# Kernel tuning notes

Hardware: AMD Instinct MI355X
Metric: run time of the kernel (lower is better)

## Reference

```python
import jax, jax.numpy as jnp
import numpy as np
from jax import lax

NF = 64
RED = 16  # CALayer / CBAM channel reduction


def conv1x1(x, w, b):
    # x: [B,Ci,H,W], w: [Co,Ci], b: [Co]
    return jnp.einsum('oi,bihw->bohw', w, x) + b[None, :, None, None]


def calayer(x, w1, b1, w2, b2):
    # SE-style channel attention (RCAN CALayer): global avg pool -> 1x1 conv -> ReLU -> 1x1 conv -> sigmoid
    y = x.mean(axis=(2, 3))                      # [B,C]
    z = jax.nn.relu(y @ w1.T + b1)               # [B,C//RED]
    s = jax.nn.sigmoid(z @ w2.T + b2)            # [B,C]
    return x * s[:, :, None, None]


def mean_variance_norm(x, eps=1e-5):
    # per-sample, per-channel spatial instance norm (AdaAttN style)
    m = x.mean(axis=(2, 3), keepdims=True)
    v = x.var(axis=(2, 3), keepdims=True)
    return (x - m) / jnp.sqrt(v + eps)


def cbam(x, mlp_w1, mlp_b1, mlp_w2, mlp_b2, sp_w, sp_b):
    # BasicAttentionBlockv1 assumed to be a CBAM block (docstring: "CBAM")
    avg = x.mean(axis=(2, 3))                    # [B,C]
    mx = x.max(axis=(2, 3))                      # [B,C]
    def mlp(v):
        return jax.nn.relu(v @ mlp_w1.T + mlp_b1) @ mlp_w2.T + mlp_b2
    s = jax.nn.sigmoid(mlp(avg) + mlp(mx))       # [B,C]
    x = x * s[:, :, None, None]
    sp_in = jnp.concatenate([x.mean(axis=1, keepdims=True), x.max(axis=1, keepdims=True)], axis=1)  # [B,2,H,W]
    m = lax.conv_general_dilated(sp_in, sp_w, (1, 1), 'SAME',
                                 dimension_numbers=('NCHW', 'OIHW', 'NCHW')) + sp_b[None, :, None, None]
    return x * jax.nn.sigmoid(m)


def setup_inputs() -> dict:
    key = jax.random.key(0)
    ks = iter(jax.random.split(key, 64))
    B, N, C, H, W = 4, 3, NF, 64, 64
    r = lambda shape, s=0.05: jax.random.normal(next(ks), shape, dtype=jnp.float32) * s
    inp = {
        'group': jax.random.normal(next(ks), (B, N, C, H, W), dtype=jnp.float32),
        'FG': jax.random.normal(next(ks), (B, N, C, H, W), dtype=jnp.float32),
        'BG': jax.random.normal(next(ks), (B, N, C, H, W), dtype=jnp.float32),
        # conv_group_1 (3nf->3nf 1x1), CALayer(3nf), conv_group_2 (3nf->nf), conv_group_3 (nf->nf)
        'wg1': r((3 * C, 3 * C)), 'bg1': r((3 * C,)),
        'cag_w1': r((3 * C // RED, 3 * C)), 'cag_b1': r((3 * C // RED,)),
        'cag_w2': r((3 * C, 3 * C // RED)), 'cag_b2': r((3 * C,)),
        'wg2': r((C, 3 * C)), 'bg2': r((C,)),
        'wg3': r((C, C)), 'bg3': r((C,)),
        # conv_center_1, CALayer(nf), conv_center_2
        'wc1': r((C, C)), 'bc1': r((C,)),
        'cac_w1': r((C // RED, C)), 'cac_b1': r((C // RED,)),
        'cac_w2': r((C, C // RED)), 'cac_b2': r((C,)),
        'wc2': r((C, C)), 'bc2': r((C,)),
        # f, g, h 1x1 convs
        'f_w': r((C, C)), 'f_b': r((C,)),
        'g_w': r((C, C)), 'g_b': r((C,)),
        'h_w': r((C, C)), 'h_b': r((C,)),
        # CBAM params
        'mlp_w1': r((C // RED, C)), 'mlp_b1': r((C // RED,)),
        'mlp_w2': r((C, C // RED)), 'mlp_b2': r((C,)),
        'sp_w': r((1, 2, 7, 7)), 'sp_b': r((1,)),
    }
    return inp


def reference(group, FG, BG,
              wg1, bg1, cag_w1, cag_b1, cag_w2, cag_b2, wg2, bg2, wg3, bg3,
              wc1, bc1, cac_w1, cac_b1, cac_w2, cac_b2, wc2, bc2,
              f_w, f_b, g_w, g_b, h_w, h_b,
              mlp_w1, mlp_b1, mlp_w2, mlp_b2, sp_w, sp_b):
    B, N, C, H, W = group.shape
    center = group[:, 1]
    FGc = FG[:, 1]
    BGc = BG[:, 1]
    grp = group.reshape(B, N * C, H, W)

    fea_group = conv1x1(grp, wg1, bg1)
    fea_group = calayer(fea_group, cag_w1, cag_b1, cag_w2, cag_b2)
    fea_group = conv1x1(fea_group, wg2, bg2)
    fea_group = conv1x1(fea_group, wg3, bg3)

    fea_center = conv1x1(center, wc1, bc1)
    fea_center = calayer(fea_center, cac_w1, cac_b1, cac_w2, cac_b2)
    fea_center = conv1x1(fea_center, wc2, bc2)

    Fq = conv1x1(fea_group, f_w, f_b).reshape(B, C, H * W).transpose(0, 2, 1)   # [B,HW,C]
    Gk = conv1x1(fea_center, g_w, g_b).reshape(B, C, H * W)                     # [B,C,HW]
    Hv = conv1x1(BGc, h_w, h_b).reshape(B, C, H * W).transpose(0, 2, 1)         # [B,HW,C]

    S = jax.nn.softmax(jnp.einsum('bqc,bck->bqk', Fq, Gk), axis=-1)             # [B,HW,HW]
    mean = jnp.einsum('bqk,bkc->bqc', S, Hv)                                    # [B,HW,C]
    second = jnp.einsum('bqk,bkc->bqc', S, Hv * Hv)
    std = jnp.sqrt(jax.nn.relu(second - mean * mean))

    mean = mean.reshape(B, H, W, C).transpose(0, 3, 1, 2)
    std = std.reshape(B, H, W, C).transpose(0, 3, 1, 2)

    transfer_FG = std * mean_variance_norm(FGc) + mean
    out = cbam(transfer_FG + BGc, mlp_w1, mlp_b1, mlp_w2, mlp_b2, sp_w, sp_b)
    return out
```

## Files before the change

kernel.cpp:

```cpp
#include <hip/hip_runtime.h>
#include <hip/hip_bf16.h>
#include <math.h>

#define HW 4096

typedef __attribute__((ext_vector_type(8))) short bf16x8;
typedef __attribute__((ext_vector_type(4))) float f32x4;

static __device__ __forceinline__ unsigned short f2bf(float x) {
    unsigned u = __float_as_uint(x);
    u += 0x7fffu + ((u >> 16) & 1u);
    return (unsigned short)(u >> 16);
}
static __device__ __forceinline__ float bf2f(unsigned short h) {
    return __uint_as_float((unsigned)h << 16);
}

__global__ __launch_bounds__(256) void k_transpose2(
    const float* __restrict__ group, const float* __restrict__ BGc, int bstride,
    unsigned short* __restrict__ X0T, unsigned short* __restrict__ BGcT)
{
    extern __shared__ float lds[];
    const int b = blockIdx.y, p0 = blockIdx.x << 6, t = threadIdx.x;
    const int z = blockIdx.z;
    const int C = z ? 64 : 192;
    const float* xb = (z ? BGc : group) + (size_t)b * bstride;
    unsigned short* outT = z ? BGcT : X0T;
    for (int idx = t; idx < (C << 6); idx += 256) {
        int c = idx >> 6, p = idx & 63;
        lds[c * 65 + p] = xb[(size_t)c * HW + p0 + p];
    }
    __syncthreads();
    unsigned short* ob = outT + ((size_t)b * HW + p0) * C;
    for (int idx = t; idx < (C << 6); idx += 256) {
        int p = idx / C, c = idx - p * C;
        ob[idx] = f2bf(lds[c * 65 + p]);
    }
}

__global__ __launch_bounds__(256) void k_xmean(
    const float* __restrict__ g, int bstride, float* __restrict__ xmean)
{
    int bc = blockIdx.x;
    int b = bc / 192, ci = bc - b * 192;
    const float* p = g + (size_t)b * bstride + (size_t)ci * HW;
    int t = threadIdx.x;
    float s = 0.f;
    for (int i = t; i < HW; i += 256) s += p[i];
    for (int o = 32; o > 0; o >>= 1) s += __shfl_down(s, o, 64);
    __shared__ float red[4];
    if ((t & 63) == 0) red[t >> 6] = s;
    __syncthreads();
    if (t == 0) xmean[bc] = (red[0] + red[1] + red[2] + red[3]) * (1.0f / HW);
}

__global__ __launch_bounds__(256) void k_mlp_compose(
    const float* __restrict__ xmean,
    const float* __restrict__ wg1, const float* __restrict__ bg1,
    const float* __restrict__ cag_w1, const float* __restrict__ cag_b1,
    const float* __restrict__ cag_w2, const float* __restrict__ cag_b2,
    const float* __restrict__ wc1, const float* __restrict__ bc1,
    const float* __restrict__ cac_w1, const float* __restrict__ cac_b1,
    const float* __restrict__ cac_w2, const float* __restrict__ cac_b2,
    const float* __restrict__ wg2, const float* __restrict__ bg2,
    const float* __restrict__ wg3, const float* __restrict__ bg3,
    const float* __restrict__ wc2, const float* __restrict__ bc2,
    const float* __restrict__ wf, const float* __restrict__ fb,
    const float* __restrict__ wgw, const float* __restrict__ gbv,
    const float* __restrict__ wh,
    unsigned short* __restrict__ WQb, float* __restrict__ biasQ,
    unsigned short* __restrict__ WKb, float* __restrict__ biasK,
    unsigned short* __restrict__ whb)
{
    const float LOG2E = 1.4426950408889634f;
    __shared__ float SM[29184];
    float* xm = SM;
    float* sg = SM + 192;
    float* sc = SM + 384;
    float* zz = SM + 448;
    float* T1 = SM + 512;
    float* Aa = SM + 4608;
    float* W1S = SM + 16896;
    float* Mm = SM + 26112;
    const int x = blockIdx.x, b = blockIdx.y, t = threadIdx.x;

    if (t < 192) xm[t] = xmean[b * 192 + t];
    __syncthreads();
    if (t < 192) {
        float a = bg1[t];
        for (int i = 0; i < 192; ++i) a = fmaf(wg1[t * 192 + i], xm[i], a);
        sg[t] = a;
    } else {
        int c = t - 192;
        float a = bc1[c];
        for (int i = 0; i < 64; ++i) a = fmaf(wc1[c * 64 + i], xm[64 + i], a);
        sc[c] = a;
    }
    __syncthreads();
    if (t < 12) {
        float a = cag_b1[t];
        for (int i = 0; i < 192; ++i) a = fmaf(cag_w1[t * 192 + i], sg[i], a);
        zz[t] = fmaxf(a, 0.f);
    }
    if (t >= 64 && t < 68) {
        int r = t - 64;
        float a = cac_b1[r];
        for (int i = 0; i < 64; ++i) a = fmaf(cac_w1[r * 64 + i], sc[i], a);
        zz[12 + r] = fmaxf(a, 0.f);
    }
    __syncthreads();
    if (t < 192) {
        float a = cag_b2[t];
        for (int j = 0; j < 12; ++j) a = fmaf(cag_w2[t * 12 + j], zz[j], a);
        sg[t] = 1.f / (1.f + __expf(-a));
    } else {
        int c = t - 192;
        float a = cac_b2[c];
        for (int j = 0; j < 4; ++j) a = fmaf(cac_w2[c * 4 + j], zz[12 + j], a);
        sc[c] = 1.f / (1.f + __expf(-a));
    }
    __syncthreads();
    float* wfS = Aa;
    float* wg3S = Aa + 4096;
    #pragma unroll
    for (int j = 0; j < 16; ++j) {
        wfS[t + j * 256] = wf[t + j * 256];
        wg3S[t + j * 256] = wg3[t + j * 256];
    }
    __syncthreads();
    #pragma unroll
    for (int j = 0; j < 16; ++j) {
        int idx = t + j * 256, o = idx >> 6, k = idx & 63;
        float a = 0.f;
        for (int m = 0; m < 64; ++m) a = fmaf(wfS[(o << 6) + m], wg3S[(m << 6) + k], a);
        T1[idx] = a;
    }
    __syncthreads();
    for (int idx = t; idx < 12288; idx += 256)
        Aa[idx] = wg2[idx] * sg[idx % 192];
    const int i0 = x * 48;
    for (int idx = t; idx < 9216; idx += 256) {
        int r = idx / 48, ii = idx - r * 48;
        W1S[idx] = wg1[r * 192 + i0 + ii];
    }
    __syncthreads();
    for (int idx = t; idx < 3072; idx += 256) {
        int o = idx / 48, ii = idx - o * 48;
        float a = 0.f;
        for (int k = 0; k < 192; ++k) a = fmaf(Aa[o * 192 + k], W1S[k * 48 + ii], a);
        Mm[idx] = a;
    }
    __syncthreads();
    for (int idx = t; idx < 3072; idx += 256) {
        int o = idx / 48, ii = idx - o * 48;
        float a = 0.f;
        for (int m = 0; m < 64; ++m) a = fmaf(T1[(o << 6) + m], Mm[m * 48 + ii], a);
        WQb[(size_t)b * 12288 + o * 192 + i0 + ii] = f2bf(a * LOG2E);
    }

    if (x == 0) {
        float* bq1 = Mm;
        float* bq2 = Mm + 64;
        float* bk1 = Mm + 128;
        __syncthreads();
        if (t < 64) {
            float a = bg2[t];
            for (int i = 0; i < 192; ++i) a = fmaf(Aa[t * 192 + i], bg1[i], a);
            bq1[t] = a;
            float c = bc2[t];
            for (int j = 0; j < 64; ++j) c = fmaf(wc2[t * 64 + j] * sc[j], bc1[j], c);
            bk1[t] = c;
        }
        __syncthreads();
        if (t < 64) {
            float a = bg3[t];
            for (int m = 0; m < 64; ++m) a = fmaf(wg3[t * 64 + m], bq1[m], a);
            bq2[t] = a;
        }
        __syncthreads();
        if (t < 64) {
            float a = fb[t];
            for (int m = 0; m < 64; ++m) a = fmaf(wf[t * 64 + m], bq2[m], a);
            biasQ[b * 64 + t] = a * LOG2E;
            float c = gbv[t];
            for (int m = 0; m < 64; ++m) c = fmaf(wgw[t * 64 + m], bk1[m], c);
            biasK[b * 64 + t] = c;
        }
        float* wc1S = Aa;
        float* wc2S = Aa + 4096;
        float* T3   = Aa + 8192;
        __syncthreads();
        #pragma unroll
        for (int j = 0; j < 16; ++j) {
            int idx = t + j * 256;
            wc1S[idx] = wc1[idx];
            wc2S[idx] = wc2[idx] * sc[idx & 63];
        }
        __syncthreads();
        #pragma unroll
        for (int j = 0; j < 16; ++j) {
            int idx = t + j * 256, m = idx >> 6, i = idx & 63;
            float a = 0.f;
            for (int k = 0; k < 64; ++k) a = fmaf(wc2S[(m << 6) + k], wc1S[(k << 6) + i], a);
            T3[idx] = a;
        }
        __syncthreads();
        #pragma unroll
        for (int j = 0; j < 16; ++j) {
            int idx = t + j * 256, o = idx >> 6, i = idx & 63;
            float a = 0.f;
            for (int m = 0; m < 64; ++m) a = fmaf(wgw[(o << 6) + m], T3[(m << 6) + i], a);
            WKb[(size_t)b * 4096 + idx] = f2bf(a);
        }
        if (b == 0) {
            #pragma unroll
            for (int j = 0; j < 16; ++j) whb[t + j * 256] = f2bf(wh[t + j * 256]);
        }
    }
}

__global__ __launch_bounds__(256) void k_proj(
    const unsigned short* __restrict__ X0T, const unsigned short* __restrict__ BGcT,
    const unsigned short* __restrict__ WQb, const float* __restrict__ biasQ,
    const unsigned short* __restrict__ WKb, const float* __restrict__ biasK,
    const unsigned short* __restrict__ whb, const float* __restrict__ h_b,
    unsigned short* __restrict__ FqT, unsigned short* __restrict__ GkT,
    unsigned short* __restrict__ hvN)
{
    const int t = threadIdx.x;
    const int w = t >> 6, lane = t & 63;
    const int gid = lane >> 4, cid = lane & 15;
    const int which = blockIdx.y;
    const int b = blockIdx.z;
    const int p0 = blockIdx.x << 6;
    const int co16 = w << 4;
    int Cin, kOff, ldx;
    const unsigned short *XT, *W;
    const float* bp;
    if (which == 0) { XT = X0T; ldx = 192; kOff = 0;  Cin = 192; W = WQb + (size_t)b * 12288; bp = biasQ + b * 64; }
    else if (which == 1) { XT = X0T; ldx = 192; kOff = 64; Cin = 64; W = WKb + (size_t)b * 4096; bp = biasK + b * 64; }
    else { XT = BGcT; ldx = 64; kOff = 0; Cin = 64; W = whb; bp = h_b; }
    const unsigned short* xrow = XT + (size_t)b * HW * ldx + kOff;
    const unsigned short* wr = W + (size_t)co16 * Cin;
    f32x4 acc[4];
    #pragma unroll
    for (int n = 0; n < 4; ++n)
        #pragma unroll
        for (int r = 0; r < 4; ++r)
            acc[n][r] = bp[co16 + 4 * gid + r];
    for (int kc = 0; kc < Cin; kc += 32) {
        bf16x8 a = *(const bf16x8*)(wr + (size_t)cid * Cin + kc + 8 * gid);
        #pragma unroll
        for (int n = 0; n < 4; ++n) {
            const unsigned short* xp = xrow + (size_t)(p0 + 16 * n + cid) * ldx + kc + 8 * gid;
            bf16x8 bfr = *(const bf16x8*)xp;
            acc[n] = __builtin_amdgcn_mfma_f32_16x16x32_bf16(a, bfr, acc[n], 0, 0, 0);
        }
    }
    #pragma unroll
    for (int n = 0; n < 4; ++n)
        #pragma unroll
        for (int r = 0; r < 4; ++r) {
            float v = acc[n][r];
            int co = co16 + 4 * gid + r;
            int p  = p0 + 16 * n + cid;
            if (which == 0)      FqT[((size_t)b * HW + p) * 64 + co] = f2bf(v);
            else if (which == 1) GkT[((size_t)b * HW + p) * 64 + co] = f2bf(v);
            else                 hvN[((size_t)b * 64 + co) * HW + p] = f2bf(v);
        }
}

__global__ __launch_bounds__(512, 2) void k_attn(
    const unsigned short* __restrict__ FqT, const unsigned short* __restrict__ GkT,
    const unsigned short* __restrict__ HvN,
    float* __restrict__ mb, float* __restrict__ sbuf)
{
    __shared__ __align__(16) char smem[65536];
    const int t = threadIdx.x;
    const int bid = blockIdx.x;
    const int b = (bid & 7) >> 1;
    const int qbase = (((bid >> 3) << 1) | (bid & 1)) << 6;
    const int w = t >> 6, lane = t & 63;
    const int gid = lane >> 4, cid = lane & 15;
    const size_t CQ = (size_t)HW * 64;
    const unsigned short* fqt = FqT + (size_t)b * CQ;
    const unsigned short* gkt = GkT + (size_t)b * CQ;
    const unsigned short* hv  = HvN + (size_t)b * CQ;
    unsigned short* Pw = (unsigned short*)smem + w * 4096;

    bf16x8 fqa[4][2];
    #pragma unroll
    for (int qt = 0; qt < 4; ++qt) {
        const unsigned short* fr = fqt + (size_t)(qbase + 16 * qt + cid) * 64 + 8 * gid;
        fqa[qt][0] = *(const bf16x8*)fr;
        fqa[qt][1] = *(const bf16x8*)(fr + 32);
    }
    bf16x8 ones;
    #pragma unroll
    for (int j = 0; j < 8; ++j) ones[j] = (short)0x3F80;

    const f32x4 fz = {0.f, 0.f, 0.f, 0.f};
    f32x4 am[4][4], a2[4][4], lac[4];
    #pragma unroll
    for (int qt = 0; qt < 4; ++qt) {
        lac[qt] = fz;
        #pragma unroll
        for (int n = 0; n < 4; ++n) { am[qt][n] = fz; a2[qt][n] = fz; }
    }

    const int k00 = w << 9;
    for (int it = 0; it < 8; ++it) {
        const int k0 = k00 + (it << 6);
        #pragma unroll
        for (int n = 0; n < 4; ++n) {
            const unsigned short* gr = gkt + (size_t)(k0 + 16 * n + cid) * 64 + 8 * gid;
            bf16x8 b0 = *(const bf16x8*)gr;
            bf16x8 b1 = *(const bf16x8*)(gr + 32);
            const int k = 16 * n + cid;
            #pragma unroll
            for (int qt = 0; qt < 4; ++qt) {
                f32x4 s = __builtin_amdgcn_mfma_f32_16x16x32_bf16(fqa[qt][0], b0, fz, 0, 0, 0);
                s = __builtin_amdgcn_mfma_f32_16x16x32_bf16(fqa[qt][1], b1, s, 0, 0, 0);
                #pragma unroll
                for (int r = 0; r < 4; ++r) {
                    int q = 4 * gid + r;
                    Pw[qt * 1024 + q * 64 + (((k >> 3) ^ (q & 7)) << 3) + (k & 7)] =
                        f2bf(__builtin_amdgcn_exp2f(s[r]));
                }
            }
        }
        bf16x8 pa[4][2];
        #pragma unroll
        for (int qt = 0; qt < 4; ++qt)
            #pragma unroll
            for (int kh = 0; kh < 2; ++kh)
                pa[qt][kh] = *(const bf16x8*)(Pw + qt * 1024 + cid * 64 +
                                              (((4 * kh + gid) ^ (cid & 7)) << 3));
        #pragma unroll
        for (int qt = 0; qt < 4; ++qt) {
            lac[qt] = __builtin_amdgcn_mfma_f32_16x16x32_bf16(pa[qt][0], ones, lac[qt], 0, 0, 0);
            lac[qt] = __builtin_amdgcn_mfma_f32_16x16x32_bf16(pa[qt][1], ones, lac[qt], 0, 0, 0);
        }
        #pragma unroll
        for (int n = 0; n < 4; ++n) {
            const unsigned short* hr = hv + (size_t)(16 * n + cid) * HW + k0;
            #pragma unroll
            for (int kh = 0; kh < 2; ++kh) {
                bf16x8 hb = *(const bf16x8*)(hr + 32 * kh + 8 * gid);
                bf16x8 h2;
                #pragma unroll
                for (int j = 0; j < 8; ++j) {
                    float v = bf2f((unsigned short)hb[j]);
                    h2[j] = (short)f2bf(v * v);
                }
                #pragma unroll
                for (int qt = 0; qt < 4; ++qt) {
                    am[qt][n] = __builtin_amdgcn_mfma_f32_16x16x32_bf16(pa[qt][kh], hb, am[qt][n], 0, 0, 0);
                    a2[qt][n] = __builtin_amdgcn_mfma_f32_16x16x32_bf16(pa[qt][kh], h2, a2[qt][n], 0, 0, 0);
                }
            }
        }
    }

    __syncthreads();
    float* lb = (float*)smem;
    #pragma unroll
    for (int qt = 0; qt < 4; ++qt)
        *(f32x4*)(lb + ((size_t)(w * 4 + qt) * 64 + lane) * 4) = lac[qt];
    __syncthreads();
    float* Lm = (float*)(smem + 32768);
    if (t < 256) {
        int qt = t >> 6, ls = t & 63;
        f32x4 s = fz;
        #pragma unroll
        for (int ww = 0; ww < 8; ++ww)
            s += *(const f32x4*)(lb + ((size_t)(ww * 4 + qt) * 64 + ls) * 4);
        *(f32x4*)(Lm + ((size_t)qt * 64 + ls) * 4) = s;
    }
    __syncthreads();
    float* ab = (float*)smem;
    f32x4 meanv = fz;
    for (int qt = 0; qt < 4; ++qt) {
        #pragma unroll
        for (int n = 0; n < 4; ++n)
            *(f32x4*)(ab + ((size_t)(w * 4 + n) * 64 + lane) * 4) = am[qt][n];
        __syncthreads();
        if (t < 256) {
            int n = t >> 6, ls = t & 63;
            f32x4 s = fz;
            #pragma unroll
            for (int ww = 0; ww < 8; ++ww)
                s += *(const f32x4*)(ab + ((size_t)(ww * 4 + n) * 64 + ls) * 4);
            f32x4 lv = *(const f32x4*)(Lm + ((size_t)qt * 64 + ls) * 4);
            #pragma unroll
            for (int r = 0; r < 4; ++r) meanv[r] = s[r] / lv[r];
            int q0s = qbase + 16 * qt + 4 * (ls >> 4);
            int c   = 16 * n + (ls & 15);
            *(f32x4*)(mb + (size_t)b * CQ + (size_t)c * HW + q0s) = meanv;
        }
        __syncthreads();
        #pragma unroll
        for (int n = 0; n < 4; ++n)
            *(f32x4*)(ab + ((size_t)(w * 4 + n) * 64 + lane) * 4) = a2[qt][n];
        __syncthreads();
        if (t < 256) {
            int n = t >> 6, ls = t & 63;
            f32x4 s = fz;
            #pragma unroll
            for (int ww = 0; ww < 8; ++ww)
                s += *(const f32x4*)(ab + ((size_t)(ww * 4 + n) * 64 + ls) * 4);
            f32x4 lv = *(const f32x4*)(Lm + ((size_t)qt * 64 + ls) * 4);
            f32x4 sv;
            #pragma unroll
            for (int r = 0; r < 4; ++r) {
                float sec = s[r] / lv[r];
                sv[r] = sqrtf(fmaxf(sec - meanv[r] * meanv[r], 0.f));
            }
            int q0s = qbase + 16 * qt + 4 * (ls >> 4);
            int c   = 16 * n + (ls & 15);
            *(f32x4*)(sbuf + (size_t)b * CQ + (size_t)c * HW + q0s) = sv;
        }
        __syncthreads();
    }
}

__global__ __launch_bounds__(256) void k_transfer_f(
    const float* __restrict__ mb, const float* __restrict__ sb,
    const float* __restrict__ FG, const float* __restrict__ BG, int bstride,
    float* __restrict__ xb, float* __restrict__ pavg, float* __restrict__ pmaxb)
{
    __shared__ float fgl[4096];
    __shared__ float r1[4], r2[4];
    const int bc = blockIdx.x, t = threadIdx.x;
    const int b = bc >> 6, c = bc & 63;
    const size_t row = (size_t)bc * HW;
    const float* fg = FG + (size_t)b * bstride + (size_t)(64 + c) * HW;
    const float* bg = BG + (size_t)b * bstride + (size_t)(64 + c) * HW;
    float s = 0.f, s2 = 0.f;
    #pragma unroll
    for (int j = 0; j < 16; ++j) {
        int i = t + j * 256;
        float v = fg[i];
        fgl[i] = v;
        s += v; s2 += v * v;
    }
    #pragma unroll
    for (int o = 32; o > 0; o >>= 1) { s += __shfl_down(s, o, 64); s2 += __shfl_down(s2, o, 64); }
    if ((t & 63) == 0) { r1[t >> 6] = s; r2[t >> 6] = s2; }
    __syncthreads();
    float m  = (r1[0] + r1[1] + r1[2] + r1[3]) * (1.0f / HW);
    float e2 = (r2[0] + r2[1] + r2[2] + r2[3]) * (1.0f / HW);
    float rs = rsqrtf(fmaxf(e2 - m * m, 0.f) + 1e-5f);
    float psum = 0.f, pmax = -1e30f;
    #pragma unroll
    for (int j = 0; j < 16; ++j) {
        int q = t + j * 256;
        float xv = sb[row + q] * (fgl[q] - m) * rs + mb[row + q] + bg[q];
        xb[row + q] = xv;
        psum += xv; pmax = fmaxf(pmax, xv);
    }
    __syncthreads();
    #pragma unroll
    for (int o = 32; o > 0; o >>= 1) {
        psum += __shfl_down(psum, o, 64);
        pmax = fmaxf(pmax, __shfl_down(pmax, o, 64));
    }
    if ((t & 63) == 0) { r1[t >> 6] = psum; r2[t >> 6] = pmax; }
    __syncthreads();
    if (t == 0) {
        pavg[bc]  = (r1[0] + r1[1] + r1[2] + r1[3]) * (1.0f / HW);
        pmaxb[bc] = fmaxf(fmaxf(r2[0], r2[1]), fmaxf(r2[2], r2[3]));
    }
}

static __device__ __forceinline__ void cbam_scale(
    const float* __restrict__ pav, const float* __restrict__ pmx,
    const float* __restrict__ w1, const float* __restrict__ b1,
    const float* __restrict__ w2, const float* __restrict__ b2,
    int b, int t, float* scb)
{
    __shared__ float za[4], zm[4];
    if (t < 4) {
        float aa = b1[t], am = b1[t];
        for (int i = 0; i < 64; ++i) {
            aa = fmaf(w1[t * 64 + i], pav[b * 64 + i], aa);
            am = fmaf(w1[t * 64 + i], pmx[b * 64 + i], am);
        }
        za[t] = fmaxf(aa, 0.f);
        zm[t] = fmaxf(am, 0.f);
    }
    __syncthreads();
    if (t < 64) {
        float a = 2.f * b2[t];
        for (int j = 0; j < 4; ++j) a = fmaf(w2[t * 4 + j], za[j] + zm[j], a);
        scb[t] = 1.f / (1.f + __expf(-a));
    }
    __syncthreads();
}

__global__ __launch_bounds__(256) void k_sp_pool(
    const float* __restrict__ xb,
    const float* __restrict__ pav, const float* __restrict__ pmx,
    const float* __restrict__ w1, const float* __restrict__ b1,
    const float* __restrict__ w2, const float* __restrict__ b2,
    float* __restrict__ spm, float* __restrict__ spx)
{
    __shared__ float scb[64];
    const int b = blockIdx.y, t = threadIdx.x;
    cbam_scale(pav, pmx, w1, b1, w2, b2, b, t, scb);
    const int p = blockIdx.x * 256 + t;
    const float* xp = xb + (size_t)b * 262144 + p;
    float sum = 0.f, mx = -1e30f;
    for (int c = 0; c < 64; ++c) {
        float v = xp[(size_t)c * HW] * scb[c];
        sum += v;
        mx = fmaxf(mx, v);
    }
    spm[b * HW + p] = sum * (1.0f / 64.0f);
    spx[b * HW + p] = mx;
}

__global__ __launch_bounds__(256) void k_spf(
    const float* __restrict__ spm, const float* __restrict__ spx,
    const float* __restrict__ w, const float* __restrict__ bias,
    const float* __restrict__ xb,
    const float* __restrict__ pav, const float* __restrict__ pmx,
    const float* __restrict__ w1, const float* __restrict__ b1,
    const float* __restrict__ w2, const float* __restrict__ b2,
    float* __restrict__ out)
{
    __shared__ float scb[64];
    const int b = blockIdx.y, t = threadIdx.x;
    cbam_scale(pav, pmx, w1, b1, w2, b2, b, t, scb);
    const int p = blockIdx.x * 256 + t;
    const int y = p >> 6, x = p & 63;
    float acc = bias[0];
    for (int dy = 0; dy < 7; ++dy) {
        int yy = y + dy - 3;
        if (yy < 0 || yy >= 64) continue;
        for (int dx = 0; dx < 7; ++dx) {
            int xx = x + dx - 3;
            if (xx < 0 || xx >= 64) continue;
            int q = b * HW + yy * 64 + xx;
            acc = fmaf(spm[q], w[dy * 7 + dx],      acc);
            acc = fmaf(spx[q], w[49 + dy * 7 + dx], acc);
        }
    }
    float sgm = 1.f / (1.f + __expf(-acc));
    const float* xp = xb + (size_t)b * 262144 + p;
    float* op = out + (size_t)b * 262144 + p;
    for (int c = 0; c < 64; ++c)
        op[(size_t)c * HW] = xp[(size_t)c * HW] * scb[c] * sgm;
}

extern "C" void kernel_launch(void* const* d_in, const int* in_sizes, int n_in,
                              void* d_out, int out_size, void* d_ws, size_t ws_size,
                              hipStream_t stream)
{
    const float* group  = (const float*)d_in[0];
    const float* FG     = (const float*)d_in[1];
    const float* BG     = (const float*)d_in[2];
    const float* wg1    = (const float*)d_in[3];
    const float* bg1    = (const float*)d_in[4];
    const float* cag_w1 = (const float*)d_in[5];
    const float* cag_b1 = (const float*)d_in[6];
    const float* cag_w2 = (const float*)d_in[7];
    const float* cag_b2 = (const float*)d_in[8];
    const float* wg2    = (const float*)d_in[9];
    const float* bg2    = (const float*)d_in[10];
    const float* wg3    = (const float*)d_in[11];
    const float* bg3    = (const float*)d_in[12];
    const float* wc1    = (const float*)d_in[13];
    const float* bc1    = (const float*)d_in[14];
    const float* cac_w1 = (const float*)d_in[15];
    const float* cac_b1 = (const float*)d_in[16];
    const float* cac_w2 = (const float*)d_in[17];
    const float* cac_b2 = (const float*)d_in[18];
    const float* wc2    = (const float*)d_in[19];
    const float* bc2    = (const float*)d_in[20];
    const float* f_w    = (const float*)d_in[21];
    const float* f_b    = (const float*)d_in[22];
    const float* g_w    = (const float*)d_in[23];
    const float* g_b    = (const float*)d_in[24];
    const float* h_w    = (const float*)d_in[25];
    const float* h_b    = (const float*)d_in[26];
    const float* mlp_w1 = (const float*)d_in[27];
    const float* mlp_b1 = (const float*)d_in[28];
    const float* mlp_w2 = (const float*)d_in[29];
    const float* mlp_b2 = (const float*)d_in[30];
    const float* sp_w   = (const float*)d_in[31];
    const float* sp_b   = (const float*)d_in[32];
    float* out = (float*)d_out;

    const int B = 4;
    const size_t CHW = (size_t)64 * HW;
    const int BST = (int)(3 * CHW);

    float* ws = (float*)d_ws;
    const size_t M = 1048576;
    unsigned short* X0T  = (unsigned short*)ws;
    unsigned short* BGcT = (unsigned short*)(ws + 3 * M / 2);
    unsigned short* FqT  = (unsigned short*)(ws + 2 * M);
    unsigned short* GkT  = (unsigned short*)(ws + 5 * M / 2);
    unsigned short* hvN  = (unsigned short*)(ws + 3 * M);
    float* mbuf = ws + 7 * M / 2;
    float* sbuf = ws + 9 * M / 2;
    float* xb   = ws + 2 * M;
    float* smalls = ws + 11 * M / 2;
    float* xmean = smalls;
    float* pav   = smalls + 1024;
    float* pmx   = smalls + 1280;
    float* biasQ = smalls + 1536;
    float* biasK = smalls + 1792;
    float* spm   = smalls + 2048;
    float* spx   = smalls + 18432;
    unsigned short* wsh = (unsigned short*)(smalls + 34816);
    unsigned short* WQb = wsh;
    unsigned short* WKb = wsh + 49152;
    unsigned short* whb = wsh + 65536;

    dim3 blk(256);

    k_transpose2<<<dim3(64, B, 2), blk, 192 * 65 * 4, stream>>>(group, BG + CHW, BST, X0T, BGcT);
    k_xmean<<<B * 192, blk, 0, stream>>>(group, BST, xmean);
    k_mlp_compose<<<dim3(4, B), blk, 0, stream>>>(
        xmean, wg1, bg1, cag_w1, cag_b1, cag_w2, cag_b2,
        wc1, bc1, cac_w1, cac_b1, cac_w2, cac_b2,
        wg2, bg2, wg3, bg3, wc2, bc2,
        f_w, f_b, g_w, g_b, h_w,
        WQb, biasQ, WKb, biasK, whb);
    k_proj<<<dim3(64, 3, B), blk, 0, stream>>>(
        X0T, BGcT, WQb, biasQ, WKb, biasK, whb, h_b, FqT, GkT, hvN);
    k_attn<<<256, 512, 0, stream>>>(FqT, GkT, hvN, mbuf, sbuf);
    k_transfer_f<<<B * 64, blk, 0, stream>>>(mbuf, sbuf, FG, BG, BST, xb, pav, pmx);
    k_sp_pool<<<dim3(HW / 256, B), blk, 0, stream>>>(xb, pav, pmx, mlp_w1, mlp_b1, mlp_w2, mlp_b2, spm, spx);
    k_spf<<<dim3(HW / 256, B), blk, 0, stream>>>(spm, spx, sp_w, sp_b, xb, pav, pmx, mlp_w1, mlp_b1, mlp_w2, mlp_b2, out);
}
```

Baseline: 187.4 us.

## Split weight composition; apply conv_group_1 as separate MFMA GEMM on activations

Measured after the change: 164.5 us (median of 3 runs). 1.14x faster.

```diff
diff --git a/kernel.cpp b/kernel.cpp
--- a/kernel.cpp
+++ b/kernel.cpp
@@ -14,6 +14,9 @@
 }
 static __device__ __forceinline__ float bf2f(unsigned short h) {
     return __uint_as_float((unsigned)h << 16);
+}
+static __device__ __forceinline__ float g4(const float4& v, int k) {
+    return k == 0 ? v.x : k == 1 ? v.y : k == 2 ? v.z : v.w;
 }
 
 __global__ __launch_bounds__(256) void k_transpose2(
@@ -46,6 +49,7 @@
     const float* p = g + (size_t)b * bstride + (size_t)ci * HW;
     int t = threadIdx.x;
     float s = 0.f;
+    #pragma unroll 4
     for (int i = t; i < HW; i += 256) s += p[i];
     for (int o = 32; o > 0; o >>= 1) s += __shfl_down(s, o, 64);
     __shared__ float red[4];
@@ -54,7 +58,31 @@
     if (t == 0) xmean[bc] = (red[0] + red[1] + red[2] + red[3]) * (1.0f / HW);
 }
 
-__global__ __launch_bounds__(256) void k_mlp_compose(
+static __device__ __forceinline__ void gemm64_tile(
+    const float* A, const float* B, int t, float acc[4][4])
+{
+    const int tr = t >> 4, tc = t & 15;
+    #pragma unroll
+    for (int i = 0; i < 4; ++i)
+        #pragma unroll
+        for (int j = 0; j < 4; ++j) acc[i][j] = 0.f;
+    for (int k4 = 0; k4 < 64; k4 += 4) {
+        float4 a[4], bb[4];
+        #pragma unroll
+        for (int i = 0; i < 4; ++i) a[i]  = *(const float4*)&A[(4 * tr + i) * 68 + k4];
+        #pragma unroll
+        for (int kk = 0; kk < 4; ++kk) bb[kk] = *(const float4*)&B[(k4 + kk) * 68 + 4 * tc];
+        #pragma unroll
+        for (int i = 0; i < 4; ++i)
+            #pragma unroll
+            for (int kk = 0; kk < 4; ++kk)
+                #pragma unroll
+                for (int j = 0; j < 4; ++j)
+                    acc[i][j] = fmaf(g4(a[i], kk), g4(bb[kk], j), acc[i][j]);
+    }
+}
+
+__global__ __launch_bounds__(256) void k_prep(
     const float* __restrict__ xmean,
     const float* __restrict__ wg1, const float* __restrict__ bg1,
     const float* __restrict__ cag_w1, const float* __restrict__ cag_b1,
@@ -68,160 +96,241 @@
     const float* __restrict__ wf, const float* __restrict__ fb,
     const float* __restrict__ wgw, const float* __restrict__ gbv,
     const float* __restrict__ wh,
-    unsigned short* __restrict__ WQb, float* __restrict__ biasQ,
-    unsigned short* __restrict__ WKb, float* __restrict__ biasK,
-    unsigned short* __restrict__ whb)
+    float* __restrict__ W3L, float* __restrict__ Uf,
+    float* __restrict__ bQ0L, float* __restrict__ bK0,
+    float* __restrict__ sgG, float* __restrict__ scG,
+    unsigned short* __restrict__ whb, unsigned short* __restrict__ wg1b)
 {
     const float LOG2E = 1.4426950408889634f;
-    __shared__ float SM[29184];
-    float* xm = SM;
-    float* sg = SM + 192;
-    float* sc = SM + 384;
-    float* zz = SM + 448;
-    float* T1 = SM + 512;
-    float* Aa = SM + 4608;
-    float* W1S = SM + 16896;
-    float* Mm = SM + 26112;
-    const int x = blockIdx.x, b = blockIdx.y, t = threadIdx.x;
-
+    __shared__ float sA[64 * 68], sB[64 * 68], sC[64 * 68];
+    __shared__ float xm[192], pg[192], pc[64], zz[16];
+    const int bid = blockIdx.x, t = threadIdx.x;
+
+    if (bid >= 4) {
+        const int x = bid - 4;
+        #pragma unroll
+        for (int j = 0; j < 16; ++j) {
+            int idx = t + j * 256, r = idx >> 6, c = idx & 63;
+            sA[r * 68 + c] = wf[idx];
+            sB[r * 68 + c] = wg3[idx];
+        }
+        __syncthreads();
+        float acc[4][4];
+        gemm64_tile(sA, sB, t, acc);
+        {
+            const int tr = t >> 4, tc = t & 15;
+            #pragma unroll
+            for (int i = 0; i < 4; ++i)
+                #pragma unroll
+                for (int j = 0; j < 4; ++j)
+                    sC[(4 * tr + i) * 68 + 4 * tc + j] = acc[i][j];
+        }
+        __syncthreads();
+        if (x == 0 && t < 64) {
+            float a = fb[t];
+            #pragma unroll 16
+            for (int m = 0; m < 64; ++m) {
+                a = fmaf(sC[t * 68 + m], bg2[m], a);
+                a = fmaf(sA[t * 68 + m], bg3[m], a);
+            }
+            bQ0L[t] = a * LOG2E;
+        }
+        __syncthreads();
+        for (int idx = t; idx < 3072; idx += 256) {
+            int c = idx >> 6, m = idx & 63;
+            sA[c * 68 + m] = wg2[m * 192 + x * 48 + c];
+        }
+        __syncthreads();
+        {
+            const int tr = t >> 4, tc = t & 15;
+            float a2[4][3];
+            #pragma unroll
+            for (int i = 0; i < 4; ++i)
+                #pragma unroll
+                for (int j = 0; j < 3; ++j) a2[i][j] = 0.f;
+            for (int k4 = 0; k4 < 64; k4 += 4) {
+                float4 a[4], bb[3];
+                #pragma unroll
+                for (int i = 0; i < 4; ++i) a[i] = *(const float4*)&sC[(4 * tr + i) * 68 + k4];
+                #pragma unroll
+                for (int j = 0; j < 3; ++j) bb[j] = *(const float4*)&sA[(3 * tc + j) * 68 + k4];
+                #pragma unroll
+                for (int i = 0; i < 4; ++i)
+                    #pragma unroll
+                    for (int j = 0; j < 3; ++j)
+                        #pragma unroll
+                        for (int kk = 0; kk < 4; ++kk)
+                            a2[i][j] = fmaf(g4(a[i], kk), g4(bb[j], kk), a2[i][j]);
+            }
+            #pragma unroll
+            for (int i = 0; i < 4; ++i)
+                #pragma unroll
+                for (int j = 0; j < 3; ++j)
+                    W3L[(4 * tr + i) * 192 + x * 48 + 3 * tc + j] = a2[i][j] * LOG2E;
+        }
+        if (x == 1) {
+            __syncthreads();
+            #pragma unroll
+            for (int j = 0; j < 16; ++j) {
+                int idx = t + j * 256, r = idx >> 6, c = idx & 63;
+                sA[r * 68 + c] = wgw[idx];
+                sB[r * 68 + c] = wc2[idx];
+            }
+            __syncthreads();
+            float au[4][4];
+            gemm64_tile(sA, sB, t, au);
+            {
+                const int tr = t >> 4, tc = t & 15;
+                #pragma unroll
+                for (int i = 0; i < 4; ++i)
+                    #pragma unroll
+                    for (int j = 0; j < 4; ++j)
+                        Uf[(4 * tr + i) * 64 + 4 * tc + j] = au[i][j];
+            }
+            if (t < 64) {
+                float a = gbv[t];
+                #pragma unroll 16
+                for (int m = 0; m < 64; ++m) a = fmaf(sA[t * 68 + m], bc2[m], a);
+                bK0[t] = a;
+            }
+        }
+        for (int idx = t; idx < 9216; idx += 256) {
+            int g = x * 9216 + idx;
+            wg1b[g] = f2bf(wg1[g]);
+        }
+        return;
+    }
+
+    const int b = bid, w = t >> 6, lane = t & 63;
     if (t < 192) xm[t] = xmean[b * 192 + t];
     __syncthreads();
-    if (t < 192) {
-        float a = bg1[t];
-        for (int i = 0; i < 192; ++i) a = fmaf(wg1[t * 192 + i], xm[i], a);
-        sg[t] = a;
-    } else {
-        int c = t - 192;
-        float a = bc1[c];
-        for (int i = 0; i < 64; ++i) a = fmaf(wc1[c * 64 + i], xm[64 + i], a);
-        sc[c] = a;
+    for (int r = w; r < 192; r += 4) {
+        float part = 0.f;
+        #pragma unroll
+        for (int j = 0; j < 3; ++j)
+            part = fmaf(wg1[r * 192 + lane + 64 * j], xm[lane + 64 * j], part);
+        #pragma unroll
+        for (int o = 32; o > 0; o >>= 1) part += __shfl_down(part, o, 64);
+        if (lane == 0) pg[r] = part + bg1[r];
+    }
+    for (int r = w; r < 64; r += 4) {
+        float part = wc1[r * 64 + lane] * xm[64 + lane];
+        #pragma unroll
+        for (int o = 32; o > 0; o >>= 1) part += __shfl_down(part, o, 64);
+        if (lane == 0) pc[r] = part + bc1[r];
     }
     __syncthreads();
     if (t < 12) {
         float a = cag_b1[t];
-        for (int i = 0; i < 192; ++i) a = fmaf(cag_w1[t * 192 + i], sg[i], a);
+        #pragma unroll 16
+        for (int i = 0; i < 192; ++i) a = fmaf(cag_w1[t * 192 + i], pg[i], a);
         zz[t] = fmaxf(a, 0.f);
     }
     if (t >= 64 && t < 68) {
         int r = t - 64;
         float a = cac_b1[r];
-        for (int i = 0; i < 64; ++i) a = fmaf(cac_w1[r * 64 + i], sc[i], a);
+        #pragma unroll 16
+        for (int i = 0; i < 64; ++i) a = fmaf(cac_w1[r * 64 + i], pc[i], a);
         zz[12 + r] = fmaxf(a, 0.f);
     }
     __syncthreads();
     if (t < 192) {
         float a = cag_b2[t];
+        #pragma unroll
         for (int j = 0; j < 12; ++j) a = fmaf(cag_w2[t * 12 + j], zz[j], a);
-        sg[t] = 1.f / (1.f + __expf(-a));
+        sgG[b * 192 + t] = 1.f / (1.f + __expf(-a));
     } else {
         int c = t - 192;
         float a = cac_b2[c];
+        #pragma unroll
         for (int j = 0; j < 4; ++j) a = fmaf(cac_w2[c * 4 + j], zz[12 + j], a);
-        sc[c] = 1.f / (1.f + __expf(-a));
-    }
-    __syncthreads();
-    float* wfS = Aa;
-    float* wg3S = Aa + 4096;
+        scG[b * 64 + c] = 1.f / (1.f + __expf(-a));
+    }
+    if (b == 0) {
+        #pragma unroll
+        for (int j = 0; j < 16; ++j) whb[t + j * 256] = f2bf(wh[t + j * 256]);
+    }
+}
+
+__global__ __launch_bounds__(256) void k_wscale(
+    const float* __restrict__ W3L, const float* __restrict__ Uf,
+    const float* __restrict__ sgG, const float* __restrict__ scG,
+    const float* __restrict__ wc1, const float* __restrict__ bc1,
+    const float* __restrict__ bK0,
+    unsigned short* __restrict__ WQs, unsigned short* __restrict__ WKb,
+    float* __restrict__ biasK)
+{
+    const int bid = blockIdx.x, t = threadIdx.x;
+    if (bid < 192) {
+        int i = bid * 256 + t;
+        int b = i / 12288, rem = i - b * 12288;
+        int c = rem % 192;
+        WQs[i] = f2bf(W3L[rem] * sgG[b * 192 + c]);
+        return;
+    }
+    __shared__ float Usc[64 * 68], sW[64 * 68], u2[64];
+    const int b = bid - 192;
     #pragma unroll
     for (int j = 0; j < 16; ++j) {
-        wfS[t + j * 256] = wf[t + j * 256];
-        wg3S[t + j * 256] = wg3[t + j * 256];
-    }
-    __syncthreads();
-    #pragma unroll
-    for (int j = 0; j < 16; ++j) {
-        int idx = t + j * 256, o = idx >> 6, k = idx & 63;
-        float a = 0.f;
-        for (int m = 0; m < 64; ++m) a = fmaf(wfS[(o << 6) + m], wg3S[(m << 6) + k], a);
-        T1[idx] = a;
-    }
-    __syncthreads();
-    for (int idx = t; idx < 12288; idx += 256)
-        Aa[idx] = wg2[idx] * sg[idx % 192];
-    const int i0 = x * 48;
-    for (int idx = t; idx < 9216; idx += 256) {
-        int r = idx / 48, ii = idx - r * 48;
-        W1S[idx] = wg1[r * 192 + i0 + ii];
-    }
-    __syncthreads();
-    for (int idx = t; idx < 3072; idx += 256) {
-        int o = idx / 48, ii = idx - o * 48;
-        float a = 0.f;
-        for (int k = 0; k < 192; ++k) a = fmaf(Aa[o * 192 + k], W1S[k * 48 + ii], a);
-        Mm[idx] = a;
-    }
-    __syncthreads();
-    for (int idx = t; idx < 3072; idx += 256) {
-        int o = idx / 48, ii = idx - o * 48;
-        float a = 0.f;
-        for (int m = 0; m < 64; ++m) a = fmaf(T1[(o << 6) + m], Mm[m * 48 + ii], a);
-        WQb[(size_t)b * 12288 + o * 192 + i0 + ii] = f2bf(a * LOG2E);
-    }
-
-    if (x == 0) {
-        float* bq1 = Mm;
-        float* bq2 = Mm + 64;
-        float* bk1 = Mm + 128;
-        __syncthreads();
-        if (t < 64) {
-            float a = bg2[t];
-            for (int i = 0; i < 192; ++i) a = fmaf(Aa[t * 192 + i], bg1[i], a);
-            bq1[t] = a;
-            float c = bc2[t];
-            for (int j = 0; j < 64; ++j) c = fmaf(wc2[t * 64 + j] * sc[j], bc1[j], c);
-            bk1[t] = c;
-        }
-        __syncthreads();
-        if (t < 64) {
-            float a = bg3[t];
-            for (int m = 0; m < 64; ++m) a = fmaf(wg3[t * 64 + m], bq1[m], a);
-            bq2[t] = a;
-        }
-        __syncthreads();
-        if (t < 64) {
-            float a = fb[t];
-            for (int m = 0; m < 64; ++m) a = fmaf(wf[t * 64 + m], bq2[m], a);
-            biasQ[b * 64 + t] = a * LOG2E;
-            float c = gbv[t];
-            for (int m = 0; m < 64; ++m) c = fmaf(wgw[t * 64 + m], bk1[m], c);
-            biasK[b * 64 + t] = c;
-        }
-        float* wc1S = Aa;
-        float* wc2S = Aa + 4096;
-        float* T3   = Aa + 8192;
-        __syncthreads();
-        #pragma unroll
-        for (int j = 0; j < 16; ++j) {
-            int idx = t + j * 256;
-            wc1S[idx] = wc1[idx];
-            wc2S[idx] = wc2[idx] * sc[idx & 63];
-        }
-        __syncthreads();
-        #pragma unroll
-        for (int j = 0; j < 16; ++j) {
-            int idx = t + j * 256, m = idx >> 6, i = idx & 63;
-            float a = 0.f;
-            for (int k = 0; k < 64; ++k) a = fmaf(wc2S[(m << 6) + k], wc1S[(k << 6) + i], a);
-            T3[idx] = a;
-        }
-        __syncthreads();
-        #pragma unroll
-        for (int j = 0; j < 16; ++j) {
-            int idx = t + j * 256, o = idx >> 6, i = idx & 63;
-            float a = 0.f;
-            for (int m = 0; m < 64; ++m) a = fmaf(wgw[(o << 6) + m], T3[(m << 6) + i], a);
-            WKb[(size_t)b * 4096 + idx] = f2bf(a);
-        }
-        if (b == 0) {
-            #pragma unroll
-            for (int j = 0; j < 16; ++j) whb[t + j * 256] = f2bf(wh[t + j * 256]);
-        }
-    }
+        int idx = t + j * 256, r = idx >> 6, c = idx & 63;
+        Usc[r * 68 + c] = Uf[idx] * scG[b * 64 + c];
+        sW[r * 68 + c]  = wc1[idx];
+    }
+    if (t < 64) u2[t] = scG[b * 64 + t] * bc1[t];
+    __syncthreads();
+    float acc[4][4];
+    gemm64_tile(Usc, sW, t, acc);
+    const int tr = t >> 4, tc = t & 15;
+    #pragma unroll
+    for (int i = 0; i < 4; ++i)
+        #pragma unroll
+        for (int j = 0; j < 4; ++j)
+            WKb[(size_t)b * 4096 + (4 * tr + i) * 64 + 4 * tc + j] = f2bf(acc[i][j]);
+    if (t < 64) {
+        float a = bK0[t];
+        #pragma unroll 16
+        for (int m = 0; m < 64; ++m) a = fmaf(Uf[t * 64 + m], u2[m], a);
+        biasK[b * 64 + t] = a;
+    }
+}
+
+__global__ __launch_bounds__(256) void k_gconv(
+    const unsigned short* __restrict__ X0T, const unsigned short* __restrict__ wg1b,
+    const float* __restrict__ bg1, unsigned short* __restrict__ g1T)
+{
+    const int t = threadIdx.x;
+    const int w = t >> 6, lane = t & 63;
+    const int gid = lane >> 4, cid = lane & 15;
+    const int b = blockIdx.z;
+    const int p0 = blockIdx.x << 6;
+    const int co16 = ((blockIdx.y << 2) + w) << 4;
+    const unsigned short* xrow = X0T + (size_t)b * HW * 192;
+    const unsigned short* wr = wg1b + (size_t)co16 * 192;
+    f32x4 acc[4];
+    #pragma unroll
+    for (int n = 0; n < 4; ++n)
+        #pragma unroll
+        for (int r = 0; r < 4; ++r)
+            acc[n][r] = bg1[co16 + 4 * gid + r];
+    for (int kc = 0; kc < 192; kc += 32) {
+        bf16x8 a = *(const bf16x8*)(wr + (size_t)cid * 192 + kc + 8 * gid);
+        #pragma unroll
+        for (int n = 0; n < 4; ++n) {
+            bf16x8 bfr = *(const bf16x8*)(xrow + (size_t)(p0 + 16 * n + cid) * 192 + kc + 8 * gid);
+            acc[n] = __builtin_amdgcn_mfma_f32_16x16x32_bf16(a, bfr, acc[n], 0, 0, 0);
+        }
+    }
+    #pragma unroll
+    for (int n = 0; n < 4; ++n)
+        #pragma unroll
+        for (int r = 0; r < 4; ++r)
+            g1T[((size_t)b * HW + p0 + 16 * n + cid) * 192 + co16 + 4 * gid + r] = f2bf(acc[n][r]);
 }
 
 __global__ __launch_bounds__(256) void k_proj(
-    const unsigned short* __restrict__ X0T, const unsigned short* __restrict__ BGcT,
-    const unsigned short* __restrict__ WQb, const float* __restrict__ biasQ,
+    const unsigned short* __restrict__ g1T, const unsigned short* __restrict__ X0T,
+    const unsigned short* __restrict__ BGcT,
+    const unsigned short* __restrict__ WQs, const float* __restrict__ bQ0L,
     const unsigned short* __restrict__ WKb, const float* __restrict__ biasK,
     const unsigned short* __restrict__ whb, const float* __restrict__ h_b,
     unsigned short* __restrict__ FqT, unsigned short* __restrict__ GkT,
@@ -237,9 +346,9 @@
     int Cin, kOff, ldx;
     const unsigned short *XT, *W;
     const float* bp;
-    if (which == 0) { XT = X0T; ldx = 192; kOff = 0;  Cin = 192; W = WQb + (size_t)b * 12288; bp = biasQ + b * 64; }
-    else if (which == 1) { XT = X0T; ldx = 192; kOff = 64; Cin = 64; W = WKb + (size_t)b * 4096; bp = biasK + b * 64; }
-    else { XT = BGcT; ldx = 64; kOff = 0; Cin = 64; W = whb; bp = h_b; }
+    if (which == 0)      { XT = g1T;  ldx = 192; kOff = 0;  Cin = 192; W = WQs + (size_t)b * 12288; bp = bQ0L; }
+    else if (which == 1) { XT = X0T;  ldx = 192; kOff = 64; Cin = 64;  W = WKb + (size_t)b * 4096;  bp = biasK + b * 64; }
+    else                 { XT = BGcT; ldx = 64;  kOff = 0;  Cin = 64;  W = whb;                      bp = h_b; }
     const unsigned short* xrow = XT + (size_t)b * HW * ldx + kOff;
     const unsigned short* wr = W + (size_t)co16 * Cin;
     f32x4 acc[4];
@@ -252,8 +361,7 @@
         bf16x8 a = *(const bf16x8*)(wr + (size_t)cid * Cin + kc + 8 * gid);
         #pragma unroll
         for (int n = 0; n < 4; ++n) {
-            const unsigned short* xp = xrow + (size_t)(p0 + 16 * n + cid) * ldx + kc + 8 * gid;
-            bf16x8 bfr = *(const bf16x8*)xp;
+            bf16x8 bfr = *(const bf16x8*)(xrow + (size_t)(p0 + 16 * n + cid) * ldx + kc + 8 * gid);
             acc[n] = __builtin_amdgcn_mfma_f32_16x16x32_bf16(a, bfr, acc[n], 0, 0, 0);
         }
     }
@@ -482,6 +590,7 @@
     __shared__ float za[4], zm[4];
     if (t < 4) {
         float aa = b1[t], am = b1[t];
+        #pragma unroll 16
         for (int i = 0; i < 64; ++i) {
             aa = fmaf(w1[t * 64 + i], pav[b * 64 + i], aa);
             am = fmaf(w1[t * 64 + i], pmx[b * 64 + i], am);
@@ -492,6 +601,7 @@
     __syncthreads();
     if (t < 64) {
         float a = 2.f * b2[t];
+        #pragma unroll
         for (int j = 0; j < 4; ++j) a = fmaf(w2[t * 4 + j], za[j] + zm[j], a);
         scb[t] = 1.f / (1.f + __expf(-a));
     }
@@ -511,6 +621,7 @@
     const int p = blockIdx.x * 256 + t;
     const float* xp = xb + (size_t)b * 262144 + p;
     float sum = 0.f, mx = -1e30f;
+    #pragma unroll 8
     for (int c = 0; c < 64; ++c) {
         float v = xp[(size_t)c * HW] * scb[c];
         sum += v;
@@ -549,6 +660,7 @@
     float sgm = 1.f / (1.f + __expf(-acc));
     const float* xp = xb + (size_t)b * 262144 + p;
     float* op = out + (size_t)b * 262144 + p;
+    #pragma unroll 8
     for (int c = 0; c < 64; ++c)
         op[(size_t)c * HW] = xp[(size_t)c * HW] * scb[c] * sgm;
 }
@@ -600,37 +712,46 @@
     const size_t M = 1048576;
     unsigned short* X0T  = (unsigned short*)ws;
     unsigned short* BGcT = (unsigned short*)(ws + 3 * M / 2);
-    unsigned short* FqT  = (unsigned short*)(ws + 2 * M);
-    unsigned short* GkT  = (unsigned short*)(ws + 5 * M / 2);
-    unsigned short* hvN  = (unsigned short*)(ws + 3 * M);
-    float* mbuf = ws + 7 * M / 2;
-    float* sbuf = ws + 9 * M / 2;
-    float* xb   = ws + 2 * M;
-    float* smalls = ws + 11 * M / 2;
+    unsigned short* g1T  = (unsigned short*)(ws + 2 * M);
+    unsigned short* FqT  = (unsigned short*)(ws + 7 * M / 2);
+    unsigned short* GkT  = (unsigned short*)(ws + 4 * M);
+    unsigned short* hvN  = (unsigned short*)(ws + 9 * M / 2);
+    float* mbuf = ws + 5 * M;
+    float* sbuf = ws + 6 * M;
+    float* xb   = ws;
+    float* smalls = ws + 7 * M;
     float* xmean = smalls;
-    float* pav   = smalls + 1024;
-    float* pmx   = smalls + 1280;
-    float* biasQ = smalls + 1536;
-    float* biasK = smalls + 1792;
-    float* spm   = smalls + 2048;
-    float* spx   = smalls + 18432;
-    unsigned short* wsh = (unsigned short*)(smalls + 34816);
-    unsigned short* WQb = wsh;
-    unsigned short* WKb = wsh + 49152;
-    unsigned short* whb = wsh + 65536;
+    float* sgG   = smalls + 768;
+    float* scG   = smalls + 1536;
+    float* pav   = smalls + 1792;
+    float* pmx   = smalls + 2048;
+    float* biasK = smalls + 2304;
+    float* bQ0L  = smalls + 2560;
+    float* bK0   = smalls + 2624;
+    float* Uf    = smalls + 2688;
+    float* W3L   = smalls + 6784;
+    float* spm   = smalls + 19072;
+    float* spx   = smalls + 35456;
+    unsigned short* wsh = (unsigned short*)(smalls + 51840);
+    unsigned short* WQs  = wsh;
+    unsigned short* WKb  = wsh + 49152;
+    unsigned short* whb  = wsh + 65536;
+    unsigned short* wg1b = wsh + 69632;
 
     dim3 blk(256);
 
     k_transpose2<<<dim3(64, B, 2), blk, 192 * 65 * 4, stream>>>(group, BG + CHW, BST, X0T, BGcT);
     k_xmean<<<B * 192, blk, 0, stream>>>(group, BST, xmean);
-    k_mlp_compose<<<dim3(4, B), blk, 0, stream>>>(
+    k_prep<<<8, blk, 0, stream>>>(
         xmean, wg1, bg1, cag_w1, cag_b1, cag_w2, cag_b2,
         wc1, bc1, cac_w1, cac_b1, cac_w2, cac_b2,
         wg2, bg2, wg3, bg3, wc2, bc2,
         f_w, f_b, g_w, g_b, h_w,
-        WQb, biasQ, WKb, biasK, whb);
+        W3L, Uf, bQ0L, bK0, sgG, scG, whb, wg1b);
+    k_wscale<<<196, blk, 0, stream>>>(W3L, Uf, sgG, scG, wc1, bc1, bK0, WQs, WKb, biasK);
+    k_gconv<<<dim3(64, 3, B), blk, 0, stream>>>(X0T, wg1b, bg1, g1T);
     k_proj<<<dim3(64, 3, B), blk, 0, stream>>>(
-        X0T, BGcT, WQb, biasQ, WKb, biasK, whb, h_b, FqT, GkT, hvN);
+        g1T, X0T, BGcT, WQs, bQ0L, WKb, biasK, whb, h_b, FqT, GkT, hvN);
     k_attn<<<256, 512, 0, stream>>>(FqT, GkT, hvN, mbuf, sbuf);
     k_transfer_f<<<B * 64, blk, 0, stream>>>(mbuf, sbuf, FG, BG, BST, xb, pav, pmx);
     k_sp_pool<<<dim3(HW / 256, B), blk, 0, stream>>>(xb, pav, pmx, mlp_w1, mlp_b1, mlp_w2, mlp_b2, spm, spx);
```
